# Kernel optimization log

Measured on AMD Instinct MI355X. Metric: run time of the kernel, lower is better.

Reference implementation:

```python
import jax, jax.numpy as jnp
import numpy as np

N = 50000       # nodes
E = 600000      # edges
ND = 128        # node_dim
ED = 64         # edge_dim
HD = 128        # hidden_dim
EPS = 1e-5

def setup_inputs() -> dict:
    key = jax.random.key(0)
    ks = jax.random.split(key, 32)
    s = 0.05
    rn = lambda k, shp, sc=s: (jax.random.normal(k, shp, dtype=jnp.float32) * sc)
    return {
        "x": jax.random.normal(ks[0], (N, ND), dtype=jnp.float32),
        "edge_index": jax.random.randint(ks[1], (2, E), 0, N),
        "edge_attr": jax.random.normal(ks[2], (E, ED), dtype=jnp.float32),
        # edge_proj: Linear(ED, ND)
        "ep_w": rn(ks[3], (ED, ND)), "ep_b": jnp.zeros((ND,), jnp.float32),
        # gnn1: GATv2Conv(in=2*ND, out=HD, heads=2, edge_dim=ED, concat=False)
        "g1_wl": rn(ks[4], (2 * ND, 2 * HD)), "g1_wr": rn(ks[5], (2 * ND, 2 * HD)),
        "g1_we": rn(ks[6], (ED, 2 * HD)), "g1_att": rn(ks[7], (2, HD)),
        "g1_b": jnp.zeros((HD,), jnp.float32),
        "n1_g": jnp.ones((HD,), jnp.float32), "n1_b": jnp.zeros((HD,), jnp.float32),
        # gnn2: GATv2Conv(in=HD, out=HD, heads=1, edge_dim=ED, concat=False)
        "g2_wl": rn(ks[8], (HD, HD)), "g2_wr": rn(ks[9], (HD, HD)),
        "g2_we": rn(ks[10], (ED, HD)), "g2_att": rn(ks[11], (1, HD)),
        "g2_b": jnp.zeros((HD,), jnp.float32),
        "n2_g": jnp.ones((HD,), jnp.float32), "n2_b": jnp.zeros((HD,), jnp.float32),
        # classifier: Linear(2*HD+ED, HD) -> ReLU -> Linear(HD, HD//2) -> ReLU -> Linear(HD//2, 1)
        "c1_w": rn(ks[12], (2 * HD + ED, HD)), "c1_b": jnp.zeros((HD,), jnp.float32),
        "c2_w": rn(ks[13], (HD, HD // 2)), "c2_b": jnp.zeros((HD // 2,), jnp.float32),
        "c3_w": rn(ks[14], (HD // 2, 1)), "c3_b": jnp.zeros((1,), jnp.float32),
    }

def _scatter_mean(src, index, dim_size):
    tot = jax.ops.segment_sum(src, index, num_segments=dim_size)
    cnt = jax.ops.segment_sum(jnp.ones((src.shape[0],), src.dtype), index, num_segments=dim_size)
    return tot / jnp.maximum(cnt, 1.0)[:, None]

def _segment_softmax(logits, seg, n):
    m = jax.ops.segment_max(logits, seg, num_segments=n)
    m = jnp.where(jnp.isfinite(m), m, 0.0)
    e = jnp.exp(logits - m[seg])
    denom = jax.ops.segment_sum(e, seg, num_segments=n)
    return e / (denom[seg] + 1e-16)

def _gatv2(xf, src, dst, eattr, wl, wr, we, att, b, n, heads, out_c):
    # PyG GATv2: message = leaky_relu(lin_l(x_j) + lin_r(x_i) + lin_edge(e)); alpha = softmax_dst(att . m)
    xl = (xf @ wl).reshape(n, heads, out_c)
    xr = (xf @ wr).reshape(n, heads, out_c)
    ee = (eattr @ we).reshape(-1, heads, out_c)
    msg = jax.nn.leaky_relu(xl[src] + xr[dst] + ee, 0.2)     # [Ea, H, C]
    logits = jnp.einsum('ehc,hc->eh', msg, att)               # [Ea, H]
    alpha = _segment_softmax(logits, dst, n)
    out = jax.ops.segment_sum(xl[src] * alpha[:, :, None], dst, num_segments=n)
    return out.mean(axis=1) + b                               # concat=False -> head mean

def _layernorm(h, g, b):
    mu = h.mean(-1, keepdims=True)
    var = ((h - mu) ** 2).mean(-1, keepdims=True)
    return (h - mu) * jax.lax.rsqrt(var + EPS) * g + b

def reference(x, edge_index, edge_attr, ep_w, ep_b,
              g1_wl, g1_wr, g1_we, g1_att, g1_b, n1_g, n1_b,
              g2_wl, g2_wr, g2_we, g2_att, g2_b, n2_g, n2_b,
              c1_w, c1_b, c2_w, c2_b, c3_w, c3_b):
    n = x.shape[0]
    src, dst = edge_index[0], edge_index[1]
    # node features from edge aggregation
    ee = jax.nn.relu(edge_attr @ ep_w + ep_b)
    x_out = _scatter_mean(ee, src, n)
    x_in = _scatter_mean(ee, dst, n)
    x_input = jnp.concatenate([x_out, x_in], axis=1)          # [N, 2*ND]
    # PyG GATv2Conv default add_self_loops=True, fill_value='mean' over incoming edge_attr
    loop_attr = _scatter_mean(edge_attr, dst, n)
    idx = jnp.arange(n)
    src_a = jnp.concatenate([src, idx])
    dst_a = jnp.concatenate([dst, idx])
    ea_a = jnp.concatenate([edge_attr, loop_attr], axis=0)
    h1 = _gatv2(x_input, src_a, dst_a, ea_a, g1_wl, g1_wr, g1_we, g1_att, g1_b, n, 2, HD)
    h1 = jax.nn.elu(_layernorm(h1, n1_g, n1_b))               # dropout off (eval)
    h2 = _gatv2(h1, src_a, dst_a, ea_a, g2_wl, g2_wr, g2_we, g2_att, g2_b, n, 1, HD)
    h2 = jax.nn.elu(_layernorm(h2, n2_g, n2_b))
    edge_rep = jnp.concatenate([h2[src], h2[dst], edge_attr], axis=1)
    z = jax.nn.relu(edge_rep @ c1_w + c1_b)
    z = jax.nn.relu(z @ c2_w + c2_b)
    return z @ c3_w + c3_b                                    # [E, 1]
```

## Files before the change

### kernel.cpp

```cpp
#include <hip/hip_runtime.h>

constexpr int   NN  = 50000;
constexpr int   NE  = 600000;
constexpr int   EA  = NE + NN;
constexpr int   ND  = 128;
constexpr int   ED  = 64;
constexpr int   HD  = 128;

__global__ void k_hist(const int* __restrict__ src, const int* __restrict__ dst,
                       int* __restrict__ cntS, int* __restrict__ cntD)
{
    int e = blockIdx.x * 256 + threadIdx.x;
    if (e >= NE) return;
    atomicAdd(&cntS[src[e]], 1);
    atomicAdd(&cntD[dst[e]], 1);
}

__global__ __launch_bounds__(1024) void k_scan(
    const int* __restrict__ cntS, const int* __restrict__ cntD,
    int* __restrict__ rpS, int* __restrict__ rpD,
    int* __restrict__ curS, int* __restrict__ curD)
{
    __shared__ int part[1024];
    const int tid = threadIdx.x;
    constexpr int CH = (NN + 1023) / 1024;
    for (int pass = 0; pass < 2; ++pass) {
        const int* cnt = pass ? cntD : cntS;
        int* rp  = pass ? rpD  : rpS;
        int* cur = pass ? curD : curS;
        int i0 = tid * CH, i1 = (i0 + CH < NN) ? i0 + CH : NN;
        int ls = 0;
        for (int i = i0; i < i1; ++i) ls += cnt[i];
        part[tid] = ls;
        __syncthreads();
        for (int off = 1; off < 1024; off <<= 1) {
            int v = (tid >= off) ? part[tid - off] : 0;
            __syncthreads();
            part[tid] += v;
            __syncthreads();
        }
        int run = tid ? part[tid - 1] : 0;
        for (int i = i0; i < i1; ++i) { rp[i] = run; cur[i] = run; run += cnt[i]; }
        if (tid == 1023) rp[NN] = run;
        __syncthreads();
    }
}

__global__ void k_scatter(const int* __restrict__ src, const int* __restrict__ dst,
                          int* __restrict__ curS, int* __restrict__ curD,
                          int* __restrict__ eidS, int* __restrict__ eidD,
                          int* __restrict__ srcS, int* __restrict__ dstS)
{
    int e = blockIdx.x * 256 + threadIdx.x;
    if (e >= NE) return;
    int s = src[e], d = dst[e];
    eidS[atomicAdd(&curS[s], 1)] = e;
    int pd = atomicAdd(&curD[d], 1);
    eidD[pd] = e;
    srcS[pd] = s;
    dstS[pd] = d;
}

__global__ __launch_bounds__(256) void k_node_inputs(
    const float* __restrict__ eattr,
    const int* __restrict__ rpS, const int* __restrict__ eidS,
    const int* __restrict__ rpD, const int* __restrict__ eidD,
    const float* __restrict__ ep_w, const float* __restrict__ ep_b,
    float* __restrict__ x_input, float* __restrict__ loopa)
{
    const int lane = threadIdx.x & 63;
    const int n = blockIdx.x * 4 + (threadIdx.x >> 6);
    if (n >= NN) return;

    float w0r[64], w1r[64];
    #pragma unroll
    for (int k = 0; k < 64; ++k) {
        w0r[k] = ep_w[k * ND + lane];
        w1r[k] = ep_w[k * ND + 64 + lane];
    }
    const float bb0 = ep_b[lane], bb1 = ep_b[64 + lane];

    float aO0 = 0.f, aO1 = 0.f;
    const int s0 = rpS[n], s1 = rpS[n + 1];
    for (int i = s0; i < s1; ++i) {
        const int e = __builtin_amdgcn_readfirstlane(eidS[i]);
        const float* ea = eattr + (long)e * ED;
        float d0 = bb0, d1 = bb1;
        #pragma unroll
        for (int k = 0; k < 64; ++k) {
            float a = ea[k];
            d0 = fmaf(a, w0r[k], d0);
            d1 = fmaf(a, w1r[k], d1);
        }
        aO0 += fmaxf(d0, 0.f);
        aO1 += fmaxf(d1, 0.f);
    }

    float aI0 = 0.f, aI1 = 0.f, la = 0.f;
    const int d0i = rpD[n], d1i = rpD[n + 1];
    for (int i = d0i; i < d1i; ++i) {
        const int e = __builtin_amdgcn_readfirstlane(eidD[i]);
        const float* ea = eattr + (long)e * ED;
        la += ea[lane];
        float d0 = bb0, d1 = bb1;
        #pragma unroll
        for (int k = 0; k < 64; ++k) {
            float a = ea[k];
            d0 = fmaf(a, w0r[k], d0);
            d1 = fmaf(a, w1r[k], d1);
        }
        aI0 += fmaxf(d0, 0.f);
        aI1 += fmaxf(d1, 0.f);
    }

    const float invS = 1.f / (float)((s1 - s0) > 1 ? (s1 - s0) : 1);
    const float invD = 1.f / (float)((d1i - d0i) > 1 ? (d1i - d0i) : 1);
    float* xrow = x_input + (long)n * 256;
    xrow[lane]        = aO0 * invS;
    xrow[64 + lane]   = aO1 * invS;
    xrow[128 + lane]  = aI0 * invD;
    xrow[192 + lane]  = aI1 * invD;
    loopa[(long)n * ED + lane] = la * invD;
}

template<int KD, int NC>
__global__ __launch_bounds__(512) void k_gemm(const float* __restrict__ A,
                                              const float* __restrict__ W,
                                              float* __restrict__ C, int M)
{
    constexpr int CPW = NC / 8;
    __shared__ float a_lds[128][65];
    const int lane = threadIdx.x & 63;
    const int wid  = __builtin_amdgcn_readfirstlane(threadIdx.x >> 6);
    const int r0   = blockIdx.x * 128;
    const int rowA = r0 + lane;
    const int rowB = r0 + 64 + lane;

    float accA[CPW], accB[CPW];
    #pragma unroll
    for (int j = 0; j < CPW; ++j) { accA[j] = 0.f; accB[j] = 0.f; }

    for (int k0 = 0; k0 < KD; k0 += 64) {
        __syncthreads();
        for (int r = wid; r < 128; r += 8) {
            int rr = r0 + r;
            a_lds[r][lane] = (rr < M) ? A[(long)rr * KD + k0 + lane] : 0.f;
        }
        __syncthreads();
        for (int k = 0; k < 64; ++k) {
            float a1 = a_lds[lane][k];
            float a2 = a_lds[64 + lane][k];
            const float* wrow = W + (long)(k0 + k) * NC + wid * CPW;
            #pragma unroll
            for (int j = 0; j < CPW; ++j) {
                float w = wrow[j];
                accA[j] = fmaf(a1, w, accA[j]);
                accB[j] = fmaf(a2, w, accB[j]);
            }
        }
    }
    if (rowA < M) {
        float* crow = C + (long)rowA * NC + wid * CPW;
        #pragma unroll
        for (int j = 0; j < CPW; ++j) crow[j] = accA[j];
    }
    if (rowB < M) {
        float* crow = C + (long)rowB * NC + wid * CPW;
        #pragma unroll
        for (int j = 0; j < CPW; ++j) crow[j] = accB[j];
    }
}

template<int HEADS>
__global__ __launch_bounds__(256) void k_gat_logits(
    const float* __restrict__ eattr,
    const int* __restrict__ eidD, const int* __restrict__ srcS, const int* __restrict__ dstS,
    const float* __restrict__ loopa,
    const float* __restrict__ xl, const float* __restrict__ xr,
    const float* __restrict__ we, const float* __restrict__ att,
    float* __restrict__ logits)
{
    constexpr int OC    = HEADS * 128;
    constexpr int CPW   = OC / 4;
    constexpr int NPASS = CPW / 32;
    __shared__ float ea_lds[128][65];
    __shared__ float p_lds[4][128];
    const int lane = threadIdx.x & 63;
    const int wid  = __builtin_amdgcn_readfirstlane(threadIdx.x >> 6);
    const int p0   = blockIdx.x * 128;

    for (int r = wid; r < 128; r += 4) {
        int pp = p0 + r;
        float v = 0.f;
        if (pp < EA) {
            const float* ap = (pp < NE) ? (eattr + (long)eidD[pp] * ED)
                                        : (loopa + (long)(pp - NE) * ED);
            v = ap[lane];
        }
        ea_lds[r][lane] = v;
    }
    __syncthreads();

    const int pA = p0 + lane;
    const int pB = p0 + 64 + lane;
    const bool vA = (pA < EA), vB = (pB < EA);
    int sA = 0, dA = 0, sB = 0, dB = 0;
    if (vA) { if (pA < NE) { sA = srcS[pA]; dA = dstS[pA]; } else { sA = dA = pA - NE; } }
    if (vB) { if (pB < NE) { sB = srcS[pB]; dB = dstS[pB]; } else { sB = dB = pB - NE; } }
    const int c0 = wid * CPW;

    float partA = 0.f, partB = 0.f;
    for (int ps = 0; ps < NPASS; ++ps) {
        const int cc = c0 + ps * 32;
        float accA[32], accB[32];
        #pragma unroll
        for (int j = 0; j < 32; ++j) { accA[j] = 0.f; accB[j] = 0.f; }
        for (int k = 0; k < 64; ++k) {
            float a1 = ea_lds[lane][k];
            float a2 = ea_lds[64 + lane][k];
            const float* wrow = we + (long)k * OC + cc;
            #pragma unroll
            for (int j = 0; j < 32; ++j) {
                float w = wrow[j];
                accA[j] = fmaf(a1, w, accA[j]);
                accB[j] = fmaf(a2, w, accB[j]);
            }
        }
        {
            const float4* xl4 = (const float4*)(xl + (long)sA * OC + cc);
            const float4* xr4 = (const float4*)(xr + (long)dA * OC + cc);
            #pragma unroll
            for (int j4 = 0; j4 < 8; ++j4) {
                float4 a4 = xl4[j4], b4 = xr4[j4];
                float m;
                m = accA[4*j4+0] + a4.x + b4.x; m = (m > 0.f) ? m : 0.2f * m; partA = fmaf(m, att[cc+4*j4+0], partA);
                m = accA[4*j4+1] + a4.y + b4.y; m = (m > 0.f) ? m : 0.2f * m; partA = fmaf(m, att[cc+4*j4+1], partA);
                m = accA[4*j4+2] + a4.z + b4.z; m = (m > 0.f) ? m : 0.2f * m; partA = fmaf(m, att[cc+4*j4+2], partA);
                m = accA[4*j4+3] + a4.w + b4.w; m = (m > 0.f) ? m : 0.2f * m; partA = fmaf(m, att[cc+4*j4+3], partA);
            }
        }
        {
            const float4* xl4 = (const float4*)(xl + (long)sB * OC + cc);
            const float4* xr4 = (const float4*)(xr + (long)dB * OC + cc);
            #pragma unroll
            for (int j4 = 0; j4 < 8; ++j4) {
                float4 a4 = xl4[j4], b4 = xr4[j4];
                float m;
                m = accB[4*j4+0] + a4.x + b4.x; m = (m > 0.f) ? m : 0.2f * m; partB = fmaf(m, att[cc+4*j4+0], partB);
                m = accB[4*j4+1] + a4.y + b4.y; m = (m > 0.f) ? m : 0.2f * m; partB = fmaf(m, att[cc+4*j4+1], partB);
                m = accB[4*j4+2] + a4.z + b4.z; m = (m > 0.f) ? m : 0.2f * m; partB = fmaf(m, att[cc+4*j4+2], partB);
                m = accB[4*j4+3] + a4.w + b4.w; m = (m > 0.f) ? m : 0.2f * m; partB = fmaf(m, att[cc+4*j4+3], partB);
            }
        }
    }
    p_lds[wid][lane]      = partA;
    p_lds[wid][64 + lane] = partB;
    __syncthreads();

    if (wid == 0) {
        if (vA) {
            if (HEADS == 2) {
                logits[(long)pA * 2 + 0] = p_lds[0][lane] + p_lds[1][lane];
                logits[(long)pA * 2 + 1] = p_lds[2][lane] + p_lds[3][lane];
            } else {
                logits[pA] = p_lds[0][lane] + p_lds[1][lane] + p_lds[2][lane] + p_lds[3][lane];
            }
        }
        if (vB) {
            if (HEADS == 2) {
                logits[(long)pB * 2 + 0] = p_lds[0][64 + lane] + p_lds[1][64 + lane];
                logits[(long)pB * 2 + 1] = p_lds[2][64 + lane] + p_lds[3][64 + lane];
            } else {
                logits[pB] = p_lds[0][64 + lane] + p_lds[1][64 + lane] + p_lds[2][64 + lane] + p_lds[3][64 + lane];
            }
        }
    }
}

template<int HEADS>
__global__ __launch_bounds__(256) void k_gat_reduce(
    const int* __restrict__ rpD, const int* __restrict__ srcS,
    const float* __restrict__ xl, const float* __restrict__ logits,
    const float* __restrict__ bias, const float* __restrict__ g, const float* __restrict__ b,
    float* __restrict__ hout)
{
    constexpr int OC = HEADS * 128;
    const int lane = threadIdx.x & 63;
    const int n = blockIdx.x * 4 + (threadIdx.x >> 6);
    if (n >= NN) return;

    const int base = rpD[n];
    const int deg  = rpD[n + 1] - base;
    const int c    = lane * 2;

    float m0 = -1e30f, m1 = -1e30f;
    for (int i = lane; i <= deg; i += 64) {
        long pp = (i < deg) ? (long)(base + i) : (long)(NE + n);
        if (HEADS == 2) {
            float2 lg = *(const float2*)&logits[pp * 2];
            m0 = fmaxf(m0, lg.x);
            m1 = fmaxf(m1, lg.y);
        } else {
            m0 = fmaxf(m0, logits[pp]);
        }
    }
    #pragma unroll
    for (int off = 32; off; off >>= 1) {
        m0 = fmaxf(m0, __shfl_xor(m0, off));
        if (HEADS == 2) m1 = fmaxf(m1, __shfl_xor(m1, off));
    }

    float s0 = 0.f, s1 = 0.f;
    for (int i = lane; i <= deg; i += 64) {
        long pp = (i < deg) ? (long)(base + i) : (long)(NE + n);
        if (HEADS == 2) {
            float2 lg = *(const float2*)&logits[pp * 2];
            s0 += __expf(lg.x - m0);
            s1 += __expf(lg.y - m1);
        } else {
            s0 += __expf(logits[pp] - m0);
        }
    }
    #pragma unroll
    for (int off = 32; off; off >>= 1) {
        s0 += __shfl_xor(s0, off);
        if (HEADS == 2) s1 += __shfl_xor(s1, off);
    }
    const float inv0 = 1.f / (s0 + 1e-16f);
    const float inv1 = 1.f / (s1 + 1e-16f);

    float a0 = 0.f, a1 = 0.f, a2 = 0.f, a3 = 0.f;
    float e0 = 0.f, e1 = 0.f, e2 = 0.f, e3 = 0.f;
    int i = 0;
    for (; i + 1 < deg; i += 2) {
        const long pA = base + i, pB = base + i + 1;
        const int  sA = __builtin_amdgcn_readfirstlane(srcS[pA]);
        const int  sB = __builtin_amdgcn_readfirstlane(srcS[pB]);
        const float* xrA = xl + (long)sA * OC;
        const float* xrB = xl + (long)sB * OC;
        if (HEADS == 2) {
            float2 lgA = *(const float2*)&logits[pA * 2];
            float2 lgB = *(const float2*)&logits[pB * 2];
            const float wA0 = __expf(lgA.x - m0) * inv0;
            const float wA1 = __expf(lgA.y - m1) * inv1;
            const float wB0 = __expf(lgB.x - m0) * inv0;
            const float wB1 = __expf(lgB.y - m1) * inv1;
            float2 xA0 = *(const float2*)(xrA + c);
            float2 xA1 = *(const float2*)(xrA + 128 + c);
            float2 xB0 = *(const float2*)(xrB + c);
            float2 xB1 = *(const float2*)(xrB + 128 + c);
            a0 = fmaf(xA0.x, wA0, a0);  a1 = fmaf(xA0.y, wA0, a1);
            a2 = fmaf(xA1.x, wA1, a2);  a3 = fmaf(xA1.y, wA1, a3);
            e0 = fmaf(xB0.x, wB0, e0);  e1 = fmaf(xB0.y, wB0, e1);
            e2 = fmaf(xB1.x, wB1, e2);  e3 = fmaf(xB1.y, wB1, e3);
        } else {
            const float wA0 = __expf(logits[pA] - m0) * inv0;
            const float wB0 = __expf(logits[pB] - m0) * inv0;
            float2 xA0 = *(const float2*)(xrA + c);
            float2 xB0 = *(const float2*)(xrB + c);
            a0 = fmaf(xA0.x, wA0, a0);  a1 = fmaf(xA0.y, wA0, a1);
            e0 = fmaf(xB0.x, wB0, e0);  e1 = fmaf(xB0.y, wB0, e1);
        }
    }
    for (; i <= deg; ++i) {
        const bool selfE = (i == deg);
        const long pp = selfE ? (long)(NE + n) : (long)(base + i);
        const int  sN = __builtin_amdgcn_readfirstlane(selfE ? n : srcS[base + i]);
        const float* xrow = xl + (long)sN * OC;
        if (HEADS == 2) {
            float2 lg = *(const float2*)&logits[pp * 2];
            const float w0 = __expf(lg.x - m0) * inv0;
            const float w1 = __expf(lg.y - m1) * inv1;
            float2 x0 = *(const float2*)(xrow + c);
            float2 x1 = *(const float2*)(xrow + 128 + c);
            a0 = fmaf(x0.x, w0, a0);  a1 = fmaf(x0.y, w0, a1);
            a2 = fmaf(x1.x, w1, a2);  a3 = fmaf(x1.y, w1, a3);
        } else {
            const float w0 = __expf(logits[pp] - m0) * inv0;
            float2 x0 = *(const float2*)(xrow + c);
            a0 = fmaf(x0.x, w0, a0);  a1 = fmaf(x0.y, w0, a1);
        }
    }
    a0 += e0; a1 += e1; a2 += e2; a3 += e3;

    float v0, v1;
    if (HEADS == 2) { v0 = 0.5f * (a0 + a2); v1 = 0.5f * (a1 + a3); }
    else            { v0 = a0;               v1 = a1; }
    float2 bb = *(const float2*)&bias[c];
    v0 += bb.x;
    v1 += bb.y;

    float sum = v0 + v1;
    #pragma unroll
    for (int off = 32; off; off >>= 1) sum += __shfl_xor(sum, off);
    const float mu = sum * (1.f / 128.f);
    const float q0 = v0 - mu, q1 = v1 - mu;
    float vs = q0 * q0 + q1 * q1;
    #pragma unroll
    for (int off = 32; off; off >>= 1) vs += __shfl_xor(vs, off);
    const float rstd = rsqrtf(vs * (1.f / 128.f) + 1e-5f);

    float2 gg = *(const float2*)&g[c];
    float2 bv = *(const float2*)&b[c];
    float y0 = q0 * rstd * gg.x + bv.x;
    float y1 = q1 * rstd * gg.y + bv.y;
    float2 outv;
    outv.x = (y0 > 0.f) ? y0 : (__expf(y0) - 1.f);
    outv.y = (y1 > 0.f) ? y1 : (__expf(y1) - 1.f);
    *(float2*)&hout[(long)n * 128 + c] = outv;
}

__global__ __launch_bounds__(256) void k_classifier(
    const float* __restrict__ Ps, const float* __restrict__ Pd,
    const int* __restrict__ eidD, const int* __restrict__ srcS, const int* __restrict__ dstS,
    const float* __restrict__ eattr,
    const float* __restrict__ c1we, const float* __restrict__ c1b,
    const float* __restrict__ c2w, const float* __restrict__ c2b,
    const float* __restrict__ c3w, const float* __restrict__ c3b,
    float* __restrict__ out)
{
    __shared__ float smem[128 * 65];
    __shared__ float p_lds[4][64];
    const int lane = threadIdx.x & 63;
    const int wid  = __builtin_amdgcn_readfirstlane(threadIdx.x >> 6);
    const int p0   = blockIdx.x * 64;
    const int p    = p0 + lane;
    const bool val = (p < NE);
    const int c0   = wid * 32;

    for (int rr = wid; rr < 64; rr += 4) {
        int pp = p0 + rr;
        smem[rr * 65 + lane] = (pp < NE) ? eattr[(long)eidD[pp] * ED + lane] : 0.f;
    }
    __syncthreads();

    float acc[32];
    #pragma unroll
    for (int j = 0; j < 32; ++j) acc[j] = c1b[c0 + j];
    for (int k = 0; k < 64; ++k) {
        float a = smem[lane * 65 + k];
        const float* wrow = c1we + (long)k * 128 + c0;
        #pragma unroll
        for (int j = 0; j < 32; ++j) acc[j] = fmaf(a, wrow[j], acc[j]);
    }

    const int sN = val ? srcS[p] : 0;
    const int dN = val ? dstS[p] : 0;
    const float4* ps4 = (const float4*)(Ps + (long)sN * 128 + c0);
    const float4* pd4 = (const float4*)(Pd + (long)dN * 128 + c0);
    #pragma unroll
    for (int j4 = 0; j4 < 8; ++j4) {
        float4 a4 = ps4[j4], b4 = pd4[j4];
        acc[4*j4+0] += a4.x + b4.x;
        acc[4*j4+1] += a4.y + b4.y;
        acc[4*j4+2] += a4.z + b4.z;
        acc[4*j4+3] += a4.w + b4.w;
    }

    __syncthreads();
    #pragma unroll
    for (int j = 0; j < 32; ++j) smem[(c0 + j) * 65 + lane] = fmaxf(acc[j], 0.f);
    __syncthreads();

    float acc2[16];
    #pragma unroll
    for (int j = 0; j < 16; ++j) acc2[j] = c2b[wid * 16 + j];
    for (int k = 0; k < 128; ++k) {
        float a = smem[k * 65 + lane];
        const float* wrow = c2w + (long)k * 64 + wid * 16;
        #pragma unroll
        for (int j = 0; j < 16; ++j) acc2[j] = fmaf(a, wrow[j], acc2[j]);
    }
    float part = 0.f;
    #pragma unroll
    for (int j = 0; j < 16; ++j) part = fmaf(fmaxf(acc2[j], 0.f), c3w[wid * 16 + j], part);
    p_lds[wid][lane] = part;
    __syncthreads();
    if (wid == 0 && val)
        out[eidD[p]] = p_lds[0][lane] + p_lds[1][lane] + p_lds[2][lane] + p_lds[3][lane] + c3b[0];
}

extern "C" void kernel_launch(void* const* d_in, const int* in_sizes, int n_in,
                              void* d_out, int out_size, void* d_ws, size_t ws_size,
                              hipStream_t stream)
{
    const int*   edge_index = (const int*)  d_in[1];
    const float* edge_attr  = (const float*)d_in[2];
    const float* ep_w  = (const float*)d_in[3];
    const float* ep_b  = (const float*)d_in[4];
    const float* g1_wl = (const float*)d_in[5];
    const float* g1_wr = (const float*)d_in[6];
    const float* g1_we = (const float*)d_in[7];
    const float* g1_att= (const float*)d_in[8];
    const float* g1_b  = (const float*)d_in[9];
    const float* n1_g  = (const float*)d_in[10];
    const float* n1_b  = (const float*)d_in[11];
    const float* g2_wl = (const float*)d_in[12];
    const float* g2_wr = (const float*)d_in[13];
    const float* g2_we = (const float*)d_in[14];
    const float* g2_att= (const float*)d_in[15];
    const float* g2_b  = (const float*)d_in[16];
    const float* n2_g  = (const float*)d_in[17];
    const float* n2_b  = (const float*)d_in[18];
    const float* c1_w  = (const float*)d_in[19];
    const float* c1_b  = (const float*)d_in[20];
    const float* c2_w  = (const float*)d_in[21];
    const float* c2_b  = (const float*)d_in[22];
    const float* c3_w  = (const float*)d_in[23];
    const float* c3_b  = (const float*)d_in[24];
    const int* src = edge_index;
    const int* dst = edge_index + NE;

    char* wsb = (char*)d_ws;
    size_t o = 0;
    auto alloc = [&](size_t bytes) { void* p = wsb + o; o += (bytes + 255) & ~(size_t)255; return p; };
    int* cntS = (int*)alloc(NN * 4);
    int* cntD = (int*)alloc(NN * 4);
    int* curS = (int*)alloc(NN * 4);
    int* curD = (int*)alloc(NN * 4);
    int* rpS  = (int*)alloc((NN + 1) * 4);
    int* rpD  = (int*)alloc((NN + 1) * 4);
    int* eidS = (int*)alloc((size_t)NE * 4);
    int* eidD = (int*)alloc((size_t)NE * 4);
    int* srcS = (int*)alloc((size_t)NE * 4);
    int* dstS = (int*)alloc((size_t)NE * 4);
    float* loopa   = (float*)alloc((size_t)NN * 64 * 4);
    float* x_input = (float*)alloc((size_t)NN * 256 * 4);
    float* xl1     = (float*)alloc((size_t)NN * 256 * 4);
    float* xr1     = (float*)alloc((size_t)NN * 256 * 4);
    float* logits  = (float*)alloc((size_t)EA * 2 * 4);
    float* h1      = (float*)alloc((size_t)NN * 128 * 4);
    float* xl2 = xl1;
    float* xr2 = xr1;
    float* h2  = x_input;
    float* Ps  = xl1;
    float* Pd  = xr1;

    hipMemsetAsync(d_ws, 0, 2 * ((NN * 4 + 255) & ~255), stream);
    k_hist<<<(NE + 255) / 256, 256, 0, stream>>>(src, dst, cntS, cntD);
    k_scan<<<1, 1024, 0, stream>>>(cntS, cntD, rpS, rpD, curS, curD);
    k_scatter<<<(NE + 255) / 256, 256, 0, stream>>>(src, dst, curS, curD, eidS, eidD, srcS, dstS);

    k_node_inputs<<<(NN + 3) / 4, 256, 0, stream>>>(edge_attr, rpS, eidS, rpD, eidD,
                                                    ep_w, ep_b, x_input, loopa);

    k_gemm<256, 256><<<(NN + 127) / 128, 512, 0, stream>>>(x_input, g1_wl, xl1, NN);
    k_gemm<256, 256><<<(NN + 127) / 128, 512, 0, stream>>>(x_input, g1_wr, xr1, NN);
    k_gat_logits<2><<<(EA + 127) / 128, 256, 0, stream>>>(edge_attr, eidD, srcS, dstS, loopa,
                                                          xl1, xr1, g1_we, g1_att, logits);
    k_gat_reduce<2><<<(NN + 3) / 4, 256, 0, stream>>>(rpD, srcS, xl1, logits, g1_b, n1_g, n1_b, h1);

    k_gemm<128, 128><<<(NN + 127) / 128, 512, 0, stream>>>(h1, g2_wl, xl2, NN);
    k_gemm<128, 128><<<(NN + 127) / 128, 512, 0, stream>>>(h1, g2_wr, xr2, NN);
    k_gat_logits<1><<<(EA + 127) / 128, 256, 0, stream>>>(edge_attr, eidD, srcS, dstS, loopa,
                                                          xl2, xr2, g2_we, g2_att, logits);
    k_gat_reduce<1><<<(NN + 3) / 4, 256, 0, stream>>>(rpD, srcS, xl2, logits, g2_b, n2_g, n2_b, h2);

    k_gemm<128, 128><<<(NN + 127) / 128, 512, 0, stream>>>(h2, c1_w,             Ps, NN);
    k_gemm<128, 128><<<(NN + 127) / 128, 512, 0, stream>>>(h2, c1_w + 128 * 128, Pd, NN);
    k_classifier<<<(NE + 63) / 64, 256, 0, stream>>>(Ps, Pd, eidD, srcS, dstS, edge_attr,
                                                     c1_w + 256 * 128, c1_b, c2_w, c2_b, c3_w, c3_b,
                                                     (float*)d_out);
}
```

Baseline: 2.094 ms.

## Materialize dst-sorted edge attributes once and reuse across all edge kernels

Adds a gather kernel that copies edge_attr into a dst-sorted contiguous buffer, with self-loop mean attributes appended at the end. Node aggregation, both GAT logits kernels and the classifier then read rows contiguously instead of gathering through eidD. The source-side aggregation uses a new src-to-dst position map in place of the eidS index list. This trades an extra 150MB copy pass for coalesced, indirection-free reads in several later kernels.

```diff
diff --git a/kernel.cpp b/kernel.cpp
--- a/kernel.cpp
+++ b/kernel.cpp
@@ -48,25 +48,35 @@
 
 __global__ void k_scatter(const int* __restrict__ src, const int* __restrict__ dst,
                           int* __restrict__ curS, int* __restrict__ curD,
-                          int* __restrict__ eidS, int* __restrict__ eidD,
+                          int* __restrict__ eidD, int* __restrict__ mapSD,
                           int* __restrict__ srcS, int* __restrict__ dstS)
 {
     int e = blockIdx.x * 256 + threadIdx.x;
     if (e >= NE) return;
     int s = src[e], d = dst[e];
-    eidS[atomicAdd(&curS[s], 1)] = e;
+    int ps = atomicAdd(&curS[s], 1);
     int pd = atomicAdd(&curD[d], 1);
     eidD[pd] = e;
+    mapSD[ps] = pd;
     srcS[pd] = s;
     dstS[pd] = d;
 }
 
-__global__ __launch_bounds__(256) void k_node_inputs(
-    const float* __restrict__ eattr,
-    const int* __restrict__ rpS, const int* __restrict__ eidS,
-    const int* __restrict__ rpD, const int* __restrict__ eidD,
+__global__ void k_build_eaD(const float* __restrict__ eattr, const int* __restrict__ eidD,
+                            float* __restrict__ eaD)
+{
+    long idx = (long)blockIdx.x * 256 + threadIdx.x;
+    int row = (int)(idx >> 6);
+    int col = (int)(idx & 63);
+    eaD[idx] = eattr[(long)eidD[row] * ED + col];
+}
+
+__global__ __launch_bounds__(256) void k_node_agg(
+    const float* __restrict__ eaDc,
+    const int* __restrict__ rpS, const int* __restrict__ mapSD,
+    const int* __restrict__ rpD,
     const float* __restrict__ ep_w, const float* __restrict__ ep_b,
-    float* __restrict__ x_input, float* __restrict__ loopa)
+    float* __restrict__ x_input, float* __restrict__ eaD_self)
 {
     const int lane = threadIdx.x & 63;
     const int n = blockIdx.x * 4 + (threadIdx.x >> 6);
@@ -83,8 +93,8 @@
     float aO0 = 0.f, aO1 = 0.f;
     const int s0 = rpS[n], s1 = rpS[n + 1];
     for (int i = s0; i < s1; ++i) {
-        const int e = __builtin_amdgcn_readfirstlane(eidS[i]);
-        const float* ea = eattr + (long)e * ED;
+        const int pd = __builtin_amdgcn_readfirstlane(mapSD[i]);
+        const float* ea = eaDc + (long)pd * ED;
         float d0 = bb0, d1 = bb1;
         #pragma unroll
         for (int k = 0; k < 64; ++k) {
@@ -99,8 +109,7 @@
     float aI0 = 0.f, aI1 = 0.f, la = 0.f;
     const int d0i = rpD[n], d1i = rpD[n + 1];
     for (int i = d0i; i < d1i; ++i) {
-        const int e = __builtin_amdgcn_readfirstlane(eidD[i]);
-        const float* ea = eattr + (long)e * ED;
+        const float* ea = eaDc + (long)i * ED;
         la += ea[lane];
         float d0 = bb0, d1 = bb1;
         #pragma unroll
@@ -120,7 +129,7 @@
     xrow[64 + lane]   = aO1 * invS;
     xrow[128 + lane]  = aI0 * invD;
     xrow[192 + lane]  = aI1 * invD;
-    loopa[(long)n * ED + lane] = la * invD;
+    eaD_self[(long)(NE + n) * ED + lane] = la * invD;
 }
 
 template<int KD, int NC>
@@ -173,9 +182,8 @@
 
 template<int HEADS>
 __global__ __launch_bounds__(256) void k_gat_logits(
-    const float* __restrict__ eattr,
-    const int* __restrict__ eidD, const int* __restrict__ srcS, const int* __restrict__ dstS,
-    const float* __restrict__ loopa,
+    const float* __restrict__ eaD,
+    const int* __restrict__ srcS, const int* __restrict__ dstS,
     const float* __restrict__ xl, const float* __restrict__ xr,
     const float* __restrict__ we, const float* __restrict__ att,
     float* __restrict__ logits)
@@ -191,13 +199,7 @@
 
     for (int r = wid; r < 128; r += 4) {
         int pp = p0 + r;
-        float v = 0.f;
-        if (pp < EA) {
-            const float* ap = (pp < NE) ? (eattr + (long)eidD[pp] * ED)
-                                        : (loopa + (long)(pp - NE) * ED);
-            v = ap[lane];
-        }
-        ea_lds[r][lane] = v;
+        ea_lds[r][lane] = (pp < EA) ? eaD[(long)pp * ED + lane] : 0.f;
     }
     __syncthreads();
 
@@ -413,7 +415,7 @@
 __global__ __launch_bounds__(256) void k_classifier(
     const float* __restrict__ Ps, const float* __restrict__ Pd,
     const int* __restrict__ eidD, const int* __restrict__ srcS, const int* __restrict__ dstS,
-    const float* __restrict__ eattr,
+    const float* __restrict__ eaD,
     const float* __restrict__ c1we, const float* __restrict__ c1b,
     const float* __restrict__ c2w, const float* __restrict__ c2b,
     const float* __restrict__ c3w, const float* __restrict__ c3b,
@@ -430,7 +432,7 @@
 
     for (int rr = wid; rr < 64; rr += 4) {
         int pp = p0 + rr;
-        smem[rr * 65 + lane] = (pp < NE) ? eattr[(long)eidD[pp] * ED + lane] : 0.f;
+        smem[rr * 65 + lane] = (pp < NE) ? eaD[(long)pp * ED + lane] : 0.f;
     }
     __syncthreads();
 
@@ -520,11 +522,11 @@
     int* curD = (int*)alloc(NN * 4);
     int* rpS  = (int*)alloc((NN + 1) * 4);
     int* rpD  = (int*)alloc((NN + 1) * 4);
-    int* eidS = (int*)alloc((size_t)NE * 4);
     int* eidD = (int*)alloc((size_t)NE * 4);
+    int* mapSD= (int*)alloc((size_t)NE * 4);
     int* srcS = (int*)alloc((size_t)NE * 4);
     int* dstS = (int*)alloc((size_t)NE * 4);
-    float* loopa   = (float*)alloc((size_t)NN * 64 * 4);
+    float* eaD     = (float*)alloc((size_t)EA * ED * 4);
     float* x_input = (float*)alloc((size_t)NN * 256 * 4);
     float* xl1     = (float*)alloc((size_t)NN * 256 * 4);
     float* xr1     = (float*)alloc((size_t)NN * 256 * 4);
@@ -539,26 +541,27 @@
     hipMemsetAsync(d_ws, 0, 2 * ((NN * 4 + 255) & ~255), stream);
     k_hist<<<(NE + 255) / 256, 256, 0, stream>>>(src, dst, cntS, cntD);
     k_scan<<<1, 1024, 0, stream>>>(cntS, cntD, rpS, rpD, curS, curD);
-    k_scatter<<<(NE + 255) / 256, 256, 0, stream>>>(src, dst, curS, curD, eidS, eidD, srcS, dstS);
-
-    k_node_inputs<<<(NN + 3) / 4, 256, 0, stream>>>(edge_attr, rpS, eidS, rpD, eidD,
-                                                    ep_w, ep_b, x_input, loopa);
+    k_scatter<<<(NE + 255) / 256, 256, 0, stream>>>(src, dst, curS, curD, eidD, mapSD, srcS, dstS);
+    k_build_eaD<<<(int)(((long)NE * ED) / 256), 256, 0, stream>>>(edge_attr, eidD, eaD);
+
+    k_node_agg<<<(NN + 3) / 4, 256, 0, stream>>>(eaD, rpS, mapSD, rpD,
+                                                 ep_w, ep_b, x_input, eaD);
 
     k_gemm<256, 256><<<(NN + 127) / 128, 512, 0, stream>>>(x_input, g1_wl, xl1, NN);
     k_gemm<256, 256><<<(NN + 127) / 128, 512, 0, stream>>>(x_input, g1_wr, xr1, NN);
-    k_gat_logits<2><<<(EA + 127) / 128, 256, 0, stream>>>(edge_attr, eidD, srcS, dstS, loopa,
+    k_gat_logits<2><<<(EA + 127) / 128, 256, 0, stream>>>(eaD, srcS, dstS,
                                                           xl1, xr1, g1_we, g1_att, logits);
     k_gat_reduce<2><<<(NN + 3) / 4, 256, 0, stream>>>(rpD, srcS, xl1, logits, g1_b, n1_g, n1_b, h1);
 
     k_gemm<128, 128><<<(NN + 127) / 128, 512, 0, stream>>>(h1, g2_wl, xl2, NN);
     k_gemm<128, 128><<<(NN + 127) / 128, 512, 0, stream>>>(h1, g2_wr, xr2, NN);
-    k_gat_logits<1><<<(EA + 127) / 128, 256, 0, stream>>>(edge_attr, eidD, srcS, dstS, loopa,
+    k_gat_logits<1><<<(EA + 127) / 128, 256, 0, stream>>>(eaD, srcS, dstS,
                                                           xl2, xr2, g2_we, g2_att, logits);
     k_gat_reduce<1><<<(NN + 3) / 4, 256, 0, stream>>>(rpD, srcS, xl2, logits, g2_b, n2_g, n2_b, h2);
 
     k_gemm<128, 128><<<(NN + 127) / 128, 512, 0, stream>>>(h2, c1_w,             Ps, NN);
     k_gemm<128, 128><<<(NN + 127) / 128, 512, 0, stream>>>(h2, c1_w + 128 * 128, Pd, NN);
-    k_classifier<<<(NE + 63) / 64, 256, 0, stream>>>(Ps, Pd, eidD, srcS, dstS, edge_attr,
+    k_classifier<<<(NE + 63) / 64, 256, 0, stream>>>(Ps, Pd, eidD, srcS, dstS, eaD,
                                                      c1_w + 256 * 128, c1_b, c2_w, c2_b, c3_w, c3_b,
                                                      (float*)d_out);
 }
```

New measurement: 2.255 ms. 7.7% more time.
